# Kernel optimization log

Hardware: AMD Instinct MI355X
Metric: run time of the kernel (lower is better)

The kernel has to match this reference:

```python
import jax, jax.numpy as jnp
import numpy as np

N_NODES = 100000
N_EDGES = 600000
D_FEAT = 128
N_OUT = 1


def setup_inputs() -> dict:
    key = jax.random.key(0)
    k1, k2, k3, k4 = jax.random.split(key, 4)
    node_inputs = jax.random.normal(k1, (N_NODES, D_FEAT), dtype=jnp.float32)
    r_indices = jax.random.randint(k2, (N_EDGES,), 0, N_NODES, dtype=jnp.int64)
    c_indices = jax.random.randint(k3, (N_EDGES,), 0, N_NODES, dtype=jnp.int64)
    w = jax.random.normal(k4, (D_FEAT, N_OUT), dtype=jnp.float32) * 0.05
    b = jnp.zeros((N_OUT,), dtype=jnp.float32)
    return {"node_inputs": node_inputs, "r_indices": r_indices,
            "c_indices": c_indices, "w": w, "b": b}


def reference(node_inputs, r_indices, c_indices, w, b):
    # Gather edge endpoints: [E, D]
    row_inputs = node_inputs[r_indices]
    col_inputs = node_inputs[c_indices]
    diff = jnp.abs(row_inputs - col_inputs)          # [E, D]
    out = diff @ w + b                               # [E, n_out]
    out = jnp.squeeze(out, axis=-1)                  # n_out == 1
    return out  # act is identity (default)
```

## Files before the change

### kernel.cpp

```cpp
#include <hip/hip_runtime.h>
#include <hip/hip_bf16.h>
#include <hip/hip_fp16.h>
#include <stdint.h>


#define D_FEAT 128
#define DBLK   8
#define DPB    16

typedef _Float16 h2v __attribute__((ext_vector_type(2)));

__device__ __forceinline__ float absdot(uint32_t a, uint32_t b, uint32_t w,
                                        float acc)
{
#if __has_builtin(__builtin_amdgcn_fdot2)
    const h2v av = __builtin_bit_cast(h2v, a);
    const h2v bv = __builtin_bit_cast(h2v, b);
    const h2v d  = av - bv;
    const uint32_t ad = __builtin_bit_cast(uint32_t, d) & 0x7FFF7FFFu;
    return __builtin_amdgcn_fdot2(__builtin_bit_cast(h2v, ad),
                                  __builtin_bit_cast(h2v, w), acc, false);
#else
    const float2 x = __half22float2(__builtin_bit_cast(__half2, a));
    const float2 y = __half22float2(__builtin_bit_cast(__half2, b));
    const float2 ww = __half22float2(__builtin_bit_cast(__half2, w));
    return acc + fabsf(x.x - y.x) * ww.x + fabsf(x.y - y.y) * ww.y;
#endif
}

__global__ __launch_bounds__(256) void convert_transpose(
    const float* __restrict__ src, __half* __restrict__ tbl2,
    const float* __restrict__ w, __half* __restrict__ wh, int n_nodes)
{
    if (blockIdx.x == 0 && threadIdx.x < (D_FEAT / 8)) {
        const float4* s = (const float4*)w + 2 * (size_t)threadIdx.x;
        const float4 a = s[0];
        const float4 c = s[1];
        float4 packed;
        ((__half2*)&packed)[0] = __floats2half2_rn(a.x, a.y);
        ((__half2*)&packed)[1] = __floats2half2_rn(a.z, a.w);
        ((__half2*)&packed)[2] = __floats2half2_rn(c.x, c.y);
        ((__half2*)&packed)[3] = __floats2half2_rn(c.z, c.w);
        ((float4*)wh)[threadIdx.x] = packed;
    }

    const int t = blockIdx.x * blockDim.x + threadIdx.x;
    const int n = t >> 3;
    const int k = t & (DBLK - 1);
    if (n >= n_nodes) return;

    const float4* s = (const float4*)(src + (size_t)n * D_FEAT + k * DPB);
    const float4 f0 = s[0], f1 = s[1], f2 = s[2], f3 = s[3];
    uint4 p0, p1;
    __half2* h0 = (__half2*)&p0;
    __half2* h1 = (__half2*)&p1;
    h0[0] = __floats2half2_rn(f0.x, f0.y);
    h0[1] = __floats2half2_rn(f0.z, f0.w);
    h0[2] = __floats2half2_rn(f1.x, f1.y);
    h0[3] = __floats2half2_rn(f1.z, f1.w);
    h1[0] = __floats2half2_rn(f2.x, f2.y);
    h1[1] = __floats2half2_rn(f2.z, f2.w);
    h1[2] = __floats2half2_rn(f3.x, f3.y);
    h1[3] = __floats2half2_rn(f3.z, f3.w);

    uint4* d = (uint4*)(tbl2 + ((size_t)k * n_nodes + n) * DPB);
    d[0] = p0;
    d[1] = p1;
}

__global__ __launch_bounds__(256) void gather_partial(
    const __half* __restrict__ tbl2,
    const __half* __restrict__ wh,
    const int*   __restrict__ r_idx,
    const int*   __restrict__ c_idx,
    float*       __restrict__ partial,
    int n_edges, int n_nodes)
{
    const int dblk  = blockIdx.x & (DBLK - 1);
    const int chunk = blockIdx.x >> 3;
    const int e = chunk * blockDim.x + threadIdx.x;
    if (e >= n_edges) return;

    const int r = __builtin_nontemporal_load(r_idx + e);
    const int c = __builtin_nontemporal_load(c_idx + e);

    const __half* base = tbl2 + (size_t)dblk * n_nodes * DPB;
    const uint4* rp = (const uint4*)(base + (size_t)r * DPB);
    const uint4* cp = (const uint4*)(base + (size_t)c * DPB);

    const uint4 a0 = rp[0];
    const uint4 a1 = rp[1];
    const uint4 b0 = cp[0];
    const uint4 b1 = cp[1];

    const uint4* wp = (const uint4*)(wh + dblk * DPB);
    const uint4 w0 = wp[0];
    const uint4 w1 = wp[1];

    float s0 = 0.f, s1 = 0.f;
    s0 = absdot(a0.x, b0.x, w0.x, s0);
    s0 = absdot(a0.y, b0.y, w0.y, s0);
    s0 = absdot(a0.z, b0.z, w0.z, s0);
    s0 = absdot(a0.w, b0.w, w0.w, s0);
    s1 = absdot(a1.x, b1.x, w1.x, s1);
    s1 = absdot(a1.y, b1.y, w1.y, s1);
    s1 = absdot(a1.z, b1.z, w1.z, s1);
    s1 = absdot(a1.w, b1.w, w1.w, s1);

    __builtin_nontemporal_store(s0 + s1,
                                partial + (size_t)dblk * n_edges + e);
}

__global__ __launch_bounds__(256) void reduce_partial(
    const float* __restrict__ partial, const float* __restrict__ b,
    float* __restrict__ out, int n_edges)
{
    const int q  = blockIdx.x * blockDim.x + threadIdx.x;
    const int e0 = q * 4;
    if (e0 >= n_edges) return;

    if (e0 + 4 <= n_edges) {
        const float bb = b[0];
        float4 acc = make_float4(bb, bb, bb, bb);
        #pragma unroll
        for (int k = 0; k < DBLK; ++k) {
            const float4 p =
                *(const float4*)(partial + (size_t)k * n_edges + e0);
            acc.x += p.x; acc.y += p.y; acc.z += p.z; acc.w += p.w;
        }
        *(float4*)(out + e0) = acc;
    } else {
        for (int e = e0; e < n_edges; ++e) {
            float acc = b[0];
            for (int k = 0; k < DBLK; ++k)
                acc += partial[(size_t)k * n_edges + e];
            out[e] = acc;
        }
    }
}

__global__ __launch_bounds__(256) void gather_edges_f32(
    const float* __restrict__ nodes,
    const int*   __restrict__ r_idx,
    const int*   __restrict__ c_idx,
    const float* __restrict__ w,
    const float* __restrict__ b,
    float*       __restrict__ out,
    int n_edges)
{
    const int tid  = blockIdx.x * blockDim.x + threadIdx.x;
    const int lane = tid & 31;
    const int edge = tid >> 5;
    if (edge >= n_edges) return;

    const int r = r_idx[edge];
    const int c = c_idx[edge];

    const float4 wv = ((const float4*)w)[lane];
    const float4 av = ((const float4*)(nodes + (size_t)r * D_FEAT))[lane];
    const float4 bv = ((const float4*)(nodes + (size_t)c * D_FEAT))[lane];

    float s = fabsf(av.x - bv.x) * wv.x
            + fabsf(av.y - bv.y) * wv.y
            + fabsf(av.z - bv.z) * wv.z
            + fabsf(av.w - bv.w) * wv.w;

    #pragma unroll
    for (int off = 16; off > 0; off >>= 1)
        s += __shfl_xor(s, off, 64);

    if (lane == 0)
        out[edge] = s + b[0];
}

extern "C" void kernel_launch(void* const* d_in, const int* in_sizes, int n_in,
                              void* d_out, int out_size, void* d_ws, size_t ws_size,
                              hipStream_t stream) {
    const float* nodes = (const float*)d_in[0];
    const int*   r_idx = (const int*)d_in[1];
    const int*   c_idx = (const int*)d_in[2];
    const float* w     = (const float*)d_in[3];
    const float* b     = (const float*)d_in[4];
    float*       out   = (float*)d_out;

    const int n_edges   = in_sizes[1];
    const int n_nodes_f = in_sizes[0];
    const int n_nodes   = n_nodes_f / D_FEAT;

    const size_t tbl_bytes  = (size_t)n_nodes_f * sizeof(__half);
    const size_t wh_bytes   = (size_t)D_FEAT * sizeof(__half);
    const size_t part_bytes = (size_t)DBLK * n_edges * sizeof(float);

    if (ws_size >= tbl_bytes + wh_bytes + part_bytes &&
        (n_nodes_f % D_FEAT) == 0) {
        __half* tbl2    = (__half*)d_ws;
        __half* wh      = tbl2 + (size_t)n_nodes_f;
        float*  partial = (float*)((char*)d_ws + tbl_bytes + wh_bytes);

        {
            const int total = n_nodes * DBLK;
            const int block = 256;
            const int grid  = (total + block - 1) / block;
            convert_transpose<<<grid, block, 0, stream>>>(
                nodes, tbl2, w, wh, n_nodes);
        }
        {
            const int block  = 256;
            const int chunks = (n_edges + block - 1) / block;
            const int grid   = chunks * DBLK;
            gather_partial<<<grid, block, 0, stream>>>(
                tbl2, wh, r_idx, c_idx, partial, n_edges, n_nodes);
        }
        {
            const int block = 256;
            const int quads = (n_edges + 3) / 4;
            const int grid  = (quads + block - 1) / block;
            reduce_partial<<<grid, block, 0, stream>>>(
                partial, b, out, n_edges);
        }
    } else {
        const int block = 256;
        const int grid  = (int)(((long long)n_edges * 32 + block - 1) / block);
        gather_edges_f32<<<grid, block, 0, stream>>>(
            nodes, r_idx, c_idx, w, b, out, n_edges);
    }
}
```

Measured before the change: 156.1 us.

## Fuse convert, gather and reduce into one cooperative kernel with grid syncs

```diff
diff --git a/kernel.cpp b/kernel.cpp
--- a/kernel.cpp
+++ b/kernel.cpp
@@ -1,12 +1,17 @@
 #include <hip/hip_runtime.h>
 #include <hip/hip_bf16.h>
 #include <hip/hip_fp16.h>
+#include <hip/hip_cooperative_groups.h>
 #include <stdint.h>
+
+namespace cg = cooperative_groups;
 
 
 #define D_FEAT 128
 #define DBLK   8
 #define DPB    16
+#define COOP_GRID  1024
+#define COOP_BLOCK 256
 
 typedef _Float16 h2v __attribute__((ext_vector_type(2)));
 
@@ -28,27 +33,12 @@
 #endif
 }
 
-__global__ __launch_bounds__(256) void convert_transpose(
-    const float* __restrict__ src, __half* __restrict__ tbl2,
-    const float* __restrict__ w, __half* __restrict__ wh, int n_nodes)
-{
-    if (blockIdx.x == 0 && threadIdx.x < (D_FEAT / 8)) {
-        const float4* s = (const float4*)w + 2 * (size_t)threadIdx.x;
-        const float4 a = s[0];
-        const float4 c = s[1];
-        float4 packed;
-        ((__half2*)&packed)[0] = __floats2half2_rn(a.x, a.y);
-        ((__half2*)&packed)[1] = __floats2half2_rn(a.z, a.w);
-        ((__half2*)&packed)[2] = __floats2half2_rn(c.x, c.y);
-        ((__half2*)&packed)[3] = __floats2half2_rn(c.z, c.w);
-        ((float4*)wh)[threadIdx.x] = packed;
-    }
-
-    const int t = blockIdx.x * blockDim.x + threadIdx.x;
+__device__ __forceinline__ void conv_item(int t, const float* __restrict__ src,
+                                          __half* __restrict__ tbl2,
+                                          int n_nodes)
+{
     const int n = t >> 3;
     const int k = t & (DBLK - 1);
-    if (n >= n_nodes) return;
-
     const float4* s = (const float4*)(src + (size_t)n * D_FEAT + k * DPB);
     const float4 f0 = s[0], f1 = s[1], f2 = s[2], f3 = s[3];
     uint4 p0, p1;
@@ -62,76 +52,181 @@
     h1[1] = __floats2half2_rn(f2.z, f2.w);
     h1[2] = __floats2half2_rn(f3.x, f3.y);
     h1[3] = __floats2half2_rn(f3.z, f3.w);
-
     uint4* d = (uint4*)(tbl2 + ((size_t)k * n_nodes + n) * DPB);
     d[0] = p0;
     d[1] = p1;
 }
 
-__global__ __launch_bounds__(256) void gather_partial(
-    const __half* __restrict__ tbl2,
-    const __half* __restrict__ wh,
+__device__ __forceinline__ void conv_w(const float* __restrict__ w,
+                                       __half* __restrict__ wh)
+{
+    const float4* s = (const float4*)w + 2 * (size_t)threadIdx.x;
+    const float4 a = s[0];
+    const float4 c = s[1];
+    float4 packed;
+    ((__half2*)&packed)[0] = __floats2half2_rn(a.x, a.y);
+    ((__half2*)&packed)[1] = __floats2half2_rn(a.z, a.w);
+    ((__half2*)&packed)[2] = __floats2half2_rn(c.x, c.y);
+    ((__half2*)&packed)[3] = __floats2half2_rn(c.z, c.w);
+    ((float4*)wh)[threadIdx.x] = packed;
+}
+
+__device__ __forceinline__ float pair_sum(const char* __restrict__ sbase,
+                                          const uint4 wv, int r, int c, int off16)
+{
+    const uint4 a = *(const uint4*)(sbase + (size_t)r * (DPB * 2) + off16);
+    const uint4 b = *(const uint4*)(sbase + (size_t)c * (DPB * 2) + off16);
+    float s = 0.f;
+    s = absdot(a.x, b.x, wv.x, s);
+    s = absdot(a.y, b.y, wv.y, s);
+    s = absdot(a.z, b.z, wv.z, s);
+    s = absdot(a.w, b.w, wv.w, s);
+    return s;
+}
+
+__global__ __launch_bounds__(COOP_BLOCK, 4) void fused_all(
+    const float* __restrict__ nodes,
     const int*   __restrict__ r_idx,
     const int*   __restrict__ c_idx,
+    const float* __restrict__ w,
+    const float* __restrict__ b,
+    __half*      __restrict__ tbl2,
+    __half*      __restrict__ wh,
     float*       __restrict__ partial,
+    float*       __restrict__ out,
     int n_edges, int n_nodes)
 {
-    const int dblk  = blockIdx.x & (DBLK - 1);
-    const int chunk = blockIdx.x >> 3;
-    const int e = chunk * blockDim.x + threadIdx.x;
+    cg::grid_group grid = cg::this_grid();
+    const int gid     = blockIdx.x * COOP_BLOCK + threadIdx.x;
+    const int gstride = COOP_GRID * COOP_BLOCK;
+
+    if (blockIdx.x == 0 && threadIdx.x < (D_FEAT / 8))
+        conv_w(w, wh);
+    {
+        const int total = n_nodes * DBLK;
+        for (int t = gid; t < total; t += gstride)
+            conv_item(t, nodes, tbl2, n_nodes);
+    }
+
+    grid.sync();
+
+    {
+        const int kb     = blockIdx.x & (DBLK - 1);
+        const int bchunk = blockIdx.x >> 3;
+        const int nblk   = COOP_GRID >> 3;
+        const int pair   = threadIdx.x >> 1;
+        const int h      = threadIdx.x & 1;
+        const int off16  = h * 16;
+        const int estep  = nblk * (COOP_BLOCK / 2);
+
+        const char* sbase = (const char*)(tbl2 + (size_t)kb * n_nodes * DPB);
+        const uint4 wv = *(const uint4*)(wh + kb * DPB + h * 8);
+        float* pslice = partial + (size_t)kb * n_edges;
+
+        for (int e0 = bchunk * (COOP_BLOCK / 2) + pair; e0 < n_edges;
+             e0 += 2 * estep) {
+            const int  e1 = e0 + estep;
+            const bool v1 = e1 < n_edges;
+
+            const int rA = __builtin_nontemporal_load(r_idx + e0);
+            const int cA = __builtin_nontemporal_load(c_idx + e0);
+            const int rB = v1 ? __builtin_nontemporal_load(r_idx + e1) : 0;
+            const int cB = v1 ? __builtin_nontemporal_load(c_idx + e1) : 0;
+
+            float sA = pair_sum(sbase, wv, rA, cA, off16);
+            float sB = pair_sum(sbase, wv, rB, cB, off16);
+
+            sA += __shfl_xor(sA, 1, 64);
+            sB += __shfl_xor(sB, 1, 64);
+
+            if (h == 0) {
+                __builtin_nontemporal_store(sA, pslice + e0);
+                if (v1) __builtin_nontemporal_store(sB, pslice + e1);
+            }
+        }
+    }
+
+    grid.sync();
+
+    {
+        const float bb = b[0];
+        const int quads = (n_edges + 3) >> 2;
+        for (int q = gid; q < quads; q += gstride) {
+            const int e0 = q * 4;
+            if (e0 + 4 <= n_edges) {
+                float4 acc = make_float4(bb, bb, bb, bb);
+                #pragma unroll
+                for (int k = 0; k < DBLK; ++k) {
+                    const float4 p =
+                        *(const float4*)(partial + (size_t)k * n_edges + e0);
+                    acc.x += p.x; acc.y += p.y; acc.z += p.z; acc.w += p.w;
+                }
+                *(float4*)(out + e0) = acc;
+            } else {
+                for (int e = e0; e < n_edges; ++e) {
+                    float acc = bb;
+                    for (int k = 0; k < DBLK; ++k)
+                        acc += partial[(size_t)k * n_edges + e];
+                    out[e] = acc;
+                }
+            }
+        }
+    }
+}
+
+__global__ __launch_bounds__(256) void k_convert(
+    const float* __restrict__ src, __half* __restrict__ tbl2,
+    const float* __restrict__ w, __half* __restrict__ wh, int n_nodes)
+{
+    if (blockIdx.x == 0 && threadIdx.x < (D_FEAT / 8))
+        conv_w(w, wh);
+    const int t = blockIdx.x * blockDim.x + threadIdx.x;
+    if (t < n_nodes * DBLK)
+        conv_item(t, src, tbl2, n_nodes);
+}
+
+__global__ __launch_bounds__(256) void k_gather_pair(
+    const __half* __restrict__ tbl2, const __half* __restrict__ wh,
+    const int* __restrict__ r_idx, const int* __restrict__ c_idx,
+    float* __restrict__ partial, int n_edges, int n_nodes)
+{
+    const int kb     = blockIdx.x & (DBLK - 1);
+    const int bchunk = blockIdx.x >> 3;
+    const int pair   = threadIdx.x >> 1;
+    const int h      = threadIdx.x & 1;
+    const int e      = bchunk * 128 + pair;
     if (e >= n_edges) return;
+
+    const char* sbase = (const char*)(tbl2 + (size_t)kb * n_nodes * DPB);
+    const uint4 wv = *(const uint4*)(wh + kb * DPB + h * 8);
 
     const int r = __builtin_nontemporal_load(r_idx + e);
     const int c = __builtin_nontemporal_load(c_idx + e);
-
-    const __half* base = tbl2 + (size_t)dblk * n_nodes * DPB;
-    const uint4* rp = (const uint4*)(base + (size_t)r * DPB);
-    const uint4* cp = (const uint4*)(base + (size_t)c * DPB);
-
-    const uint4 a0 = rp[0];
-    const uint4 a1 = rp[1];
-    const uint4 b0 = cp[0];
-    const uint4 b1 = cp[1];
-
-    const uint4* wp = (const uint4*)(wh + dblk * DPB);
-    const uint4 w0 = wp[0];
-    const uint4 w1 = wp[1];
-
-    float s0 = 0.f, s1 = 0.f;
-    s0 = absdot(a0.x, b0.x, w0.x, s0);
-    s0 = absdot(a0.y, b0.y, w0.y, s0);
-    s0 = absdot(a0.z, b0.z, w0.z, s0);
-    s0 = absdot(a0.w, b0.w, w0.w, s0);
-    s1 = absdot(a1.x, b1.x, w1.x, s1);
-    s1 = absdot(a1.y, b1.y, w1.y, s1);
-    s1 = absdot(a1.z, b1.z, w1.z, s1);
-    s1 = absdot(a1.w, b1.w, w1.w, s1);
-
-    __builtin_nontemporal_store(s0 + s1,
-                                partial + (size_t)dblk * n_edges + e);
-}
-
-__global__ __launch_bounds__(256) void reduce_partial(
+    float s = pair_sum(sbase, wv, r, c, h * 16);
+    s += __shfl_xor(s, 1, 64);
+    if (h == 0)
+        __builtin_nontemporal_store(s, partial + (size_t)kb * n_edges + e);
+}
+
+__global__ __launch_bounds__(256) void k_reduce(
     const float* __restrict__ partial, const float* __restrict__ b,
     float* __restrict__ out, int n_edges)
 {
     const int q  = blockIdx.x * blockDim.x + threadIdx.x;
     const int e0 = q * 4;
     if (e0 >= n_edges) return;
-
+    const float bb = b[0];
     if (e0 + 4 <= n_edges) {
-        const float bb = b[0];
         float4 acc = make_float4(bb, bb, bb, bb);
         #pragma unroll
         for (int k = 0; k < DBLK; ++k) {
-            const float4 p =
-                *(const float4*)(partial + (size_t)k * n_edges + e0);
+            const float4 p = *(const float4*)(partial + (size_t)k * n_edges + e0);
             acc.x += p.x; acc.y += p.y; acc.z += p.z; acc.w += p.w;
         }
         *(float4*)(out + e0) = acc;
     } else {
         for (int e = e0; e < n_edges; ++e) {
-            float acc = b[0];
+            float acc = bb;
             for (int k = 0; k < DBLK; ++k)
                 acc += partial[(size_t)k * n_edges + e];
             out[e] = acc;
@@ -188,35 +283,47 @@
     const int n_nodes   = n_nodes_f / D_FEAT;
 
     const size_t tbl_bytes  = (size_t)n_nodes_f * sizeof(__half);
-    const size_t wh_bytes   = (size_t)D_FEAT * sizeof(__half);
+    const size_t wh_bytes   = 256;
     const size_t part_bytes = (size_t)DBLK * n_edges * sizeof(float);
+
+    static int coop_ok = -1;
+    if (coop_ok < 0) {
+        hipDeviceProp_t prop;
+        coop_ok = (hipGetDeviceProperties(&prop, 0) == hipSuccess &&
+                   prop.cooperativeLaunch) ? 1 : 0;
+    }
 
     if (ws_size >= tbl_bytes + wh_bytes + part_bytes &&
         (n_nodes_f % D_FEAT) == 0) {
         __half* tbl2    = (__half*)d_ws;
-        __half* wh      = tbl2 + (size_t)n_nodes_f;
+        __half* wh      = (__half*)((char*)d_ws + tbl_bytes);
         float*  partial = (float*)((char*)d_ws + tbl_bytes + wh_bytes);
 
-        {
-            const int total = n_nodes * DBLK;
-            const int block = 256;
-            const int grid  = (total + block - 1) / block;
-            convert_transpose<<<grid, block, 0, stream>>>(
-                nodes, tbl2, w, wh, n_nodes);
-        }
-        {
-            const int block  = 256;
-            const int chunks = (n_edges + block - 1) / block;
-            const int grid   = chunks * DBLK;
-            gather_partial<<<grid, block, 0, stream>>>(
-                tbl2, wh, r_idx, c_idx, partial, n_edges, n_nodes);
-        }
-        {
-            const int block = 256;
-            const int quads = (n_edges + 3) / 4;
-            const int grid  = (quads + block - 1) / block;
-            reduce_partial<<<grid, block, 0, stream>>>(
-                partial, b, out, n_edges);
+        if (coop_ok) {
+            void* args[] = {
+                (void*)&nodes, (void*)&r_idx, (void*)&c_idx, (void*)&w,
+                (void*)&b, (void*)&tbl2, (void*)&wh, (void*)&partial,
+                (void*)&out, (void*)&n_edges, (void*)&n_nodes
+            };
+            hipLaunchCooperativeKernel((const void*)fused_all,
+                                       dim3(COOP_GRID), dim3(COOP_BLOCK),
+                                       args, 0, stream);
+        } else {
+            {
+                const int total = n_nodes * DBLK;
+                const int grid  = (total + 255) / 256;
+                k_convert<<<grid, 256, 0, stream>>>(nodes, tbl2, w, wh, n_nodes);
+            }
+            {
+                const int chunks = (n_edges + 127) / 128;
+                k_gather_pair<<<chunks * DBLK, 256, 0, stream>>>(
+                    tbl2, wh, r_idx, c_idx, partial, n_edges, n_nodes);
+            }
+            {
+                const int quads = (n_edges + 3) / 4;
+                const int grid  = (quads + 255) / 256;
+                k_reduce<<<grid, 256, 0, stream>>>(partial, b, out, n_edges);
+            }
         }
     } else {
         const int block = 256;
```

After: 454.3 us. 191% more time.
